# Performance work log

Measured on AMD Instinct MI355X. Metric: run time of the kernel, lower is better.

The kernel has to match this reference:

```python
import jax, jax.numpy as jnp
import numpy as np

TEMPERATURE = 0.2
EPS = 1e-12  # matches torch F.normalize eps


def _l2_normalize(x):
    n = jnp.linalg.norm(x, axis=-1, keepdims=True)
    return x / jnp.maximum(n, EPS)


def setup_inputs() -> dict:
    key = jax.random.key(0)
    k1, k2 = jax.random.split(key)
    B, D = 8192, 256
    return {
        "user_embeddings": jax.random.normal(k1, (B, D), dtype=jnp.float32),
        "positive_item_embeddings": jax.random.normal(k2, (B, D), dtype=jnp.float32),
    }


def reference(user_embeddings, positive_item_embeddings):
    # all_item_embeddings=None branch: in-batch implicit negatives.
    u = _l2_normalize(user_embeddings)            # [B, D]
    p = _l2_normalize(positive_item_embeddings)   # [B, D]
    sim = jnp.einsum("bd,nd->bn", u, p) / TEMPERATURE  # [B, B]
    pos_sim = jnp.diagonal(sim)                   # [B]; equals the torch pos_sim
    # Original concatenates pos_sim[i] with the off-diagonal row entries and takes
    # logsumexp. Since the diagonal of sim IS pos_sim[i], that set equals the full
    # row, so loss_i = -pos_sim_i + logsumexp(sim[i, :]). Vectorized over the batch.
    lse = jax.nn.logsumexp(sim, axis=1)           # [B]
    return jnp.mean(lse - pos_sim)
```

## Files before the change

### kernel.cpp

```cpp
#include <hip/hip_runtime.h>
#include <hip/hip_bf16.h>

#define DDIM 256
#define NROWS 8192

typedef __attribute__((ext_vector_type(8))) __bf16 bf16x8;
typedef __attribute__((ext_vector_type(4))) float floatx4;

__device__ __forceinline__ void async16(const void* g, void* l) {
    __builtin_amdgcn_global_load_lds(
        (const __attribute__((address_space(1))) unsigned int*)g,
        (__attribute__((address_space(3))) unsigned int*)l,
        16, 0, 0);
}

__device__ __forceinline__ float fexp2(float x) {
    float r; asm("v_exp_f32 %0, %1" : "=v"(r) : "v"(x)); return r;
}

__device__ __forceinline__ void stage_rows(const unsigned short* __restrict__ g,
                                           unsigned short* l,
                                           int wv, int lane,
                                           int rows_per_wave, int ninstr)
{
    const int lrow = lane >> 5;
    const int gcol = lane & 31;
    const int r0 = wv * rows_per_wave;
    for (int j = 0; j < ninstr; ++j) {
        const int rb = r0 + j * 2;
        const int r  = rb + lrow;
        const int gg = gcol ^ (r & 7);
        async16(g + (size_t)r * DDIM + gg * 8, l + (size_t)rb * DDIM);
    }
}

__device__ __forceinline__ bf16x8 frag(const unsigned short* base, int row,
                                       int ks, int q, int m)
{
    return *(const bf16x8*)&base[(size_t)row * DDIM
                                 + (((ks * 4 + q) ^ (m & 7)) * 8)];
}

__global__ __launch_bounds__(256) void normalize_kernel(
    const float* __restrict__ U, const float* __restrict__ P,
    unsigned short* __restrict__ Un, unsigned short* __restrict__ Pn,
    float* __restrict__ possim, float* __restrict__ rowsum,
    float* __restrict__ out, int* __restrict__ counter)
{
    if (blockIdx.x == 0 && threadIdx.x == 0) { out[0] = 0.0f; counter[0] = 0; }
    const int lane = threadIdx.x & 63;
    const int row  = blockIdx.x * 4 + (threadIdx.x >> 6);
    const size_t base = (size_t)row * DDIM + lane * 4;
    const float4 u4 = *(const float4*)(U + base);
    const float4 p4 = *(const float4*)(P + base);
    float su = u4.x*u4.x + u4.y*u4.y + u4.z*u4.z + u4.w*u4.w;
    float sp = p4.x*p4.x + p4.y*p4.y + p4.z*p4.z + p4.w*p4.w;
    float up = u4.x*p4.x + u4.y*p4.y + u4.z*p4.z + u4.w*p4.w;
    #pragma unroll
    for (int d = 1; d < 64; d <<= 1) {
        su += __shfl_xor(su, d);
        sp += __shfl_xor(sp, d);
        up += __shfl_xor(up, d);
    }
    const float iu = rsqrtf(fmaxf(su, 1e-24f));
    const float ip = rsqrtf(fmaxf(sp, 1e-24f));
    if (lane == 0) {
        possim[row] = up * iu * ip;
        rowsum[row] = 0.0f;
    }
    union { ushort4 s4; __hip_bfloat16 h[4]; } cu, cp;
    cu.h[0] = __float2bfloat16(u4.x * iu); cu.h[1] = __float2bfloat16(u4.y * iu);
    cu.h[2] = __float2bfloat16(u4.z * iu); cu.h[3] = __float2bfloat16(u4.w * iu);
    cp.h[0] = __float2bfloat16(p4.x * ip); cp.h[1] = __float2bfloat16(p4.y * ip);
    cp.h[2] = __float2bfloat16(p4.z * ip); cp.h[3] = __float2bfloat16(p4.w * ip);
    *(ushort4*)(Un + base) = cu.s4;
    *(ushort4*)(Pn + base) = cp.s4;
}

__device__ __forceinline__ void stage_tile(const unsigned short* __restrict__ Bglob,
                                           const unsigned* boff,
                                           unsigned short* lds,
                                           int t, int buf, int wv)
{
    const char* src = (const char*)Bglob + (unsigned)t * 16384u;
    char* dst = (char*)lds + buf * 16384 + wv * 4096;
    #pragma unroll
    for (int jj = 0; jj < 4; ++jj)
        async16(src + boff[jj], dst + jj * 1024);
}

template<int J>
__device__ __forceinline__ void compute_tile(const unsigned short* lds,
        const unsigned (&bb)[2][2], const bf16x8 (&afr)[2][8],
        float (&rowpart)[2][4])
{
    floatx4 acc[2][2];
    #pragma unroll
    for (int t = 0; t < 2; ++t) {
        acc[t][0] = {0.0f, 0.0f, 0.0f, 0.0f};
        acc[t][1] = {0.0f, 0.0f, 0.0f, 0.0f};
    }
    const char* base = (const char*)lds;
    #pragma unroll
    for (int ks = 0; ks < 8; ++ks) {
        const bf16x8 b0 = *(const bf16x8*)(base + bb[0][ks & 1]
                                           + (J * 16384 + (ks >> 1) * 128));
        const bf16x8 b1 = *(const bf16x8*)(base + bb[1][ks & 1]
                                           + (J * 16384 + (ks >> 1) * 128));
        #pragma unroll
        for (int t = 0; t < 2; ++t) {
            acc[t][0] = __builtin_amdgcn_mfma_f32_16x16x32_bf16(
                afr[t][ks], b0, acc[t][0], 0, 0, 0);
            acc[t][1] = __builtin_amdgcn_mfma_f32_16x16x32_bf16(
                afr[t][ks], b1, acc[t][1], 0, 0, 0);
        }
    }
    #pragma unroll
    for (int t = 0; t < 2; ++t)
        #pragma unroll
        for (int h = 0; h < 2; ++h)
            #pragma unroll
            for (int r = 0; r < 4; ++r)
                rowpart[t][r] += fexp2(acc[t][h][r] * 7.2134752044448169f);
}

__global__ __launch_bounds__(256, 2) void sim_exp_rowsum(
    const unsigned short* __restrict__ Un,
    const unsigned short* __restrict__ Pn,
    float* __restrict__ rowsum,
    const float* __restrict__ possim,
    int* __restrict__ counter,
    float* __restrict__ out)
{
    __shared__ __align__(16) unsigned short lds[32768];
    __shared__ float ws4[4];
    __shared__ int ticket_s;

    const int tid  = threadIdx.x;
    const int lane = tid & 63;
    const int wv   = tid >> 6;
    const int m = lane & 15;
    const int q = lane >> 4;

    const int stripe = blockIdx.x >> 3;
    const int oct    = blockIdx.x & 7;

    const unsigned short* Aglob = Un + (size_t)stripe * 128 * DDIM;
    stage_rows(Aglob, lds, wv, lane, 32, 16);
    __syncthreads();

    bf16x8 afr[2][8];
    #pragma unroll
    for (int t = 0; t < 2; ++t)
        #pragma unroll
        for (int ks = 0; ks < 8; ++ks)
            afr[t][ks] = frag(lds, wv * 32 + t * 16 + m, ks, q, m);
    __syncthreads();

    const int c10 = m & 3, c2 = (m >> 2) & 1;
    unsigned bb[2][2];
    #pragma unroll
    for (int h = 0; h < 2; ++h)
        #pragma unroll
        for (int par = 0; par < 2; ++par)
            bb[h][par] = (unsigned)((h * 16 + m) * 512
                                    + ((q ^ c10) << 4) + ((par ^ c2) << 6));

    const int lrow = lane >> 5, gcol = lane & 31;
    unsigned boff[4];
    #pragma unroll
    for (int jj = 0; jj < 4; ++jj) {
        const int r = wv * 8 + jj * 2 + lrow;
        const int gg = gcol ^ (r & 7);
        boff[jj] = (unsigned)(r * 512 + gg * 16);
    }

    const unsigned short* Bglob = Pn + (size_t)(oct * 1024) * DDIM;
    float rowpart[2][4] = {{0.f, 0.f, 0.f, 0.f}, {0.f, 0.f, 0.f, 0.f}};

    stage_tile(Bglob, boff, lds, 0, 0, wv);
    stage_tile(Bglob, boff, lds, 1, 1, wv);
    stage_tile(Bglob, boff, lds, 2, 2, wv);

#define SLOT(JBUF, NWAIT, DOSTAGE, STAGET)                                   \
    do {                                                                     \
        asm volatile("s_waitcnt lgkmcnt(0)" ::: "memory");                   \
        asm volatile("s_waitcnt vmcnt(" #NWAIT ")" ::: "memory");            \
        __builtin_amdgcn_s_barrier();                                        \
        if (DOSTAGE)                                                         \
            stage_tile(Bglob, boff, lds, (STAGET), (STAGET) & 3, wv);        \
        compute_tile<JBUF>(lds, bb, afr, rowpart);                           \
    } while (0)

    for (int i = 0; i < 7; ++i) {
        const int t0 = i * 4;
        SLOT(0, 8, true, t0 + 3);
        SLOT(1, 8, true, t0 + 4);
        SLOT(2, 8, true, t0 + 5);
        SLOT(3, 8, true, t0 + 6);
    }
    SLOT(0, 8, true, 31);
    SLOT(1, 8, false, 0);
    SLOT(2, 4, false, 0);
    SLOT(3, 0, false, 0);
#undef SLOT

    #pragma unroll
    for (int t = 0; t < 2; ++t) {
        #pragma unroll
        for (int r = 0; r < 4; ++r) {
            float s = rowpart[t][r];
            s += __shfl_xor(s, 1);
            s += __shfl_xor(s, 2);
            s += __shfl_xor(s, 4);
            s += __shfl_xor(s, 8);
            if (m == 0) {
                const int grow = stripe * 128 + wv * 32 + t * 16 + q * 4 + r;
                atomicAdd(&rowsum[grow], s);
            }
        }
    }

    __threadfence();
    __syncthreads();
    if (tid == 0)
        ticket_s = __hip_atomic_fetch_add(counter, 1, __ATOMIC_ACQ_REL,
                                          __HIP_MEMORY_SCOPE_AGENT);
    __syncthreads();
    if (ticket_s == 511) {
        float part = 0.0f;
        for (int i = tid; i < NROWS; i += 256) {
            const float rs = __hip_atomic_load(&rowsum[i], __ATOMIC_RELAXED,
                                               __HIP_MEMORY_SCOPE_AGENT);
            part += __logf(rs) - 5.0f * possim[i];
        }
        #pragma unroll
        for (int d = 1; d < 64; d <<= 1) part += __shfl_xor(part, d);
        if (lane == 0) ws4[wv] = part;
        __syncthreads();
        if (tid == 0)
            out[0] = (ws4[0] + ws4[1] + ws4[2] + ws4[3]) * (1.0f / (float)NROWS);
    }
}

extern "C" void kernel_launch(void* const* d_in, const int* in_sizes, int n_in,
                              void* d_out, int out_size, void* d_ws, size_t ws_size,
                              hipStream_t stream) {
    const float* U = (const float*)d_in[0];
    const float* P = (const float*)d_in[1];
    float* out = (float*)d_out;
    char* ws = (char*)d_ws;
    unsigned short* Un = (unsigned short*)ws;
    unsigned short* Pn = (unsigned short*)(ws + 4194304);
    float* rowsum = (float*)(ws + 8388608);
    float* possim = (float*)(ws + 8388608 + 32768);
    int* counter  = (int*)(ws + 8388608 + 65536);

    normalize_kernel<<<NROWS / 4, 256, 0, stream>>>(U, P, Un, Pn, possim, rowsum,
                                                    out, counter);
    sim_exp_rowsum<<<512, 256, 0, stream>>>(Un, Pn, rowsum, possim, counter, out);
}
```

Measured before the change: 149.1 us.

## Double-buffer B tiles, load A fragments directly, and launch 1024 blocks

```diff
diff --git a/kernel.cpp b/kernel.cpp
--- a/kernel.cpp
+++ b/kernel.cpp
@@ -3,6 +3,7 @@
 
 #define DDIM 256
 #define NROWS 8192
+#define NTILES 16
 
 typedef __attribute__((ext_vector_type(8))) __bf16 bf16x8;
 typedef __attribute__((ext_vector_type(4))) float floatx4;
@@ -16,29 +17,6 @@
 
 __device__ __forceinline__ float fexp2(float x) {
     float r; asm("v_exp_f32 %0, %1" : "=v"(r) : "v"(x)); return r;
-}
-
-__device__ __forceinline__ void stage_rows(const unsigned short* __restrict__ g,
-                                           unsigned short* l,
-                                           int wv, int lane,
-                                           int rows_per_wave, int ninstr)
-{
-    const int lrow = lane >> 5;
-    const int gcol = lane & 31;
-    const int r0 = wv * rows_per_wave;
-    for (int j = 0; j < ninstr; ++j) {
-        const int rb = r0 + j * 2;
-        const int r  = rb + lrow;
-        const int gg = gcol ^ (r & 7);
-        async16(g + (size_t)r * DDIM + gg * 8, l + (size_t)rb * DDIM);
-    }
-}
-
-__device__ __forceinline__ bf16x8 frag(const unsigned short* base, int row,
-                                       int ks, int q, int m)
-{
-    return *(const bf16x8*)&base[(size_t)row * DDIM
-                                 + (((ks * 4 + q) ^ (m & 7)) * 8)];
 }
 
 __global__ __launch_bounds__(256) void normalize_kernel(
@@ -124,7 +102,7 @@
                 rowpart[t][r] += fexp2(acc[t][h][r] * 7.2134752044448169f);
 }
 
-__global__ __launch_bounds__(256, 2) void sim_exp_rowsum(
+__global__ __launch_bounds__(256, 4) void sim_exp_rowsum(
     const unsigned short* __restrict__ Un,
     const unsigned short* __restrict__ Pn,
     float* __restrict__ rowsum,
@@ -132,7 +110,7 @@
     int* __restrict__ counter,
     float* __restrict__ out)
 {
-    __shared__ __align__(16) unsigned short lds[32768];
+    __shared__ __align__(16) unsigned short lds[16384];
     __shared__ float ws4[4];
     __shared__ int ticket_s;
 
@@ -142,20 +120,16 @@
     const int m = lane & 15;
     const int q = lane >> 4;
 
-    const int stripe = blockIdx.x >> 3;
-    const int oct    = blockIdx.x & 7;
-
-    const unsigned short* Aglob = Un + (size_t)stripe * 128 * DDIM;
-    stage_rows(Aglob, lds, wv, lane, 32, 16);
-    __syncthreads();
-
+    const int stripe = blockIdx.x >> 4;
+    const int cg     = blockIdx.x & 15;
+
+    const unsigned short* Arow = Un + (size_t)(stripe * 128 + wv * 32 + m) * DDIM;
     bf16x8 afr[2][8];
     #pragma unroll
     for (int t = 0; t < 2; ++t)
         #pragma unroll
         for (int ks = 0; ks < 8; ++ks)
-            afr[t][ks] = frag(lds, wv * 32 + t * 16 + m, ks, q, m);
-    __syncthreads();
+            afr[t][ks] = *(const bf16x8*)(Arow + t * 16 * DDIM + (ks * 4 + q) * 8);
 
     const int c10 = m & 3, c2 = (m >> 2) & 1;
     unsigned bb[2][2];
@@ -175,35 +149,34 @@
         boff[jj] = (unsigned)(r * 512 + gg * 16);
     }
 
-    const unsigned short* Bglob = Pn + (size_t)(oct * 1024) * DDIM;
+    const unsigned short* Bglob = Pn + (size_t)(cg * 512) * DDIM;
     float rowpart[2][4] = {{0.f, 0.f, 0.f, 0.f}, {0.f, 0.f, 0.f, 0.f}};
 
     stage_tile(Bglob, boff, lds, 0, 0, wv);
     stage_tile(Bglob, boff, lds, 1, 1, wv);
-    stage_tile(Bglob, boff, lds, 2, 2, wv);
-
-#define SLOT(JBUF, NWAIT, DOSTAGE, STAGET)                                   \
+    asm volatile("s_waitcnt vmcnt(4)" ::: "memory");
+    __builtin_amdgcn_s_barrier();
+
+#define BARSTAGE(T)                                                          \
     do {                                                                     \
         asm volatile("s_waitcnt lgkmcnt(0)" ::: "memory");                   \
-        asm volatile("s_waitcnt vmcnt(" #NWAIT ")" ::: "memory");            \
         __builtin_amdgcn_s_barrier();                                        \
-        if (DOSTAGE)                                                         \
-            stage_tile(Bglob, boff, lds, (STAGET), (STAGET) & 3, wv);        \
-        compute_tile<JBUF>(lds, bb, afr, rowpart);                           \
+        if ((T) + 2 < NTILES) {                                              \
+            stage_tile(Bglob, boff, lds, (T) + 2, (T) & 1, wv);              \
+            asm volatile("s_waitcnt vmcnt(4)" ::: "memory");                 \
+        } else {                                                             \
+            asm volatile("s_waitcnt vmcnt(0)" ::: "memory");                 \
+        }                                                                    \
+        __builtin_amdgcn_s_barrier();                                        \
     } while (0)
 
-    for (int i = 0; i < 7; ++i) {
-        const int t0 = i * 4;
-        SLOT(0, 8, true, t0 + 3);
-        SLOT(1, 8, true, t0 + 4);
-        SLOT(2, 8, true, t0 + 5);
-        SLOT(3, 8, true, t0 + 6);
-    }
-    SLOT(0, 8, true, 31);
-    SLOT(1, 8, false, 0);
-    SLOT(2, 4, false, 0);
-    SLOT(3, 0, false, 0);
-#undef SLOT
+    for (int t = 0; t < NTILES; t += 2) {
+        compute_tile<0>(lds, bb, afr, rowpart);
+        BARSTAGE(t);
+        compute_tile<1>(lds, bb, afr, rowpart);
+        if (t + 2 < NTILES) BARSTAGE(t + 1);
+    }
+#undef BARSTAGE
 
     #pragma unroll
     for (int t = 0; t < 2; ++t) {
@@ -227,7 +200,7 @@
         ticket_s = __hip_atomic_fetch_add(counter, 1, __ATOMIC_ACQ_REL,
                                           __HIP_MEMORY_SCOPE_AGENT);
     __syncthreads();
-    if (ticket_s == 511) {
+    if (ticket_s == 1023) {
         float part = 0.0f;
         for (int i = tid; i < NROWS; i += 256) {
             const float rs = __hip_atomic_load(&rowsum[i], __ATOMIC_RELAXED,
@@ -258,5 +231,5 @@
 
     normalize_kernel<<<NROWS / 4, 256, 0, stream>>>(U, P, Un, Pn, possim, rowsum,
                                                     out, counter);
-    sim_exp_rowsum<<<512, 256, 0, stream>>>(Un, Pn, rowsum, possim, counter, out);
-}
+    sim_exp_rowsum<<<1024, 256, 0, stream>>>(Un, Pn, rowsum, possim, counter, out);
+}
```

Measured after the change: 180.2 us. 1.21x slower.
